# Kernel tuning notes

Measured on AMD Instinct MI355X. Metric: run time of the kernel, lower is better.

The kernel has to match this reference:

```python
import jax, jax.numpy as jnp
import numpy as np

NO_EDGE_OFFSET_T_NORM = 10.0
NO_EDGE_OFFSET_T_CONORM = -10.0

B, I, O = 64, 1024, 1024  # num_samples, in_features, out_features
N_EDGE_TYPES = 3          # 0=no_edge, 1=edge (identity), 2=negation (1-x)
N_OP_TYPES = 2            # 0=T_Norm.min, 1=T_Conorm.max


def setup_inputs() -> dict:
    key = jax.random.key(0)
    k1, k2, k3, k4 = jax.random.split(key, 4)
    # fuzzy inputs in [0, 1]
    x = jax.random.uniform(k1, (B, I), dtype=jnp.float32)
    # operator_type_counts is all-ones -> uniform multinomial over operator types (per node)
    op_idx = jax.random.randint(k2, (O,), 0, N_OP_TYPES, dtype=jnp.int32)
    # edge_type_count is all-ones -> uniform multinomial over edge types,
    # resampled per (sample, node, edge) exactly as the double python loop does
    et = jax.random.randint(k3, (B, O, I), 0, N_EDGE_TYPES, dtype=jnp.int32)
    # source fix-up: if every sampled index is 0 (all no_edge), force one random edge to type 1
    all_zero = jnp.all(et == 0, axis=-1)                      # [B, O]
    rand_pos = jax.random.randint(k4, (B, O), 0, I, dtype=jnp.int32)
    force = all_zero[:, :, None] & (jnp.arange(I)[None, None, :] == rand_pos[:, :, None])
    et = jnp.where(force, 1, et)
    return {"x": x, "edge_type_idx": et, "op_idx": op_idx}


def reference(x, edge_type_idx, op_idx):
    # x: [B, I] float; edge_type_idx: [B, O, I] int; op_idx: [O] int
    is_tnorm = (op_idx == 0)                                   # [O], op 0 = min (T_Norm)
    xb = x[:, None, :]                                         # [B, 1, I]
    # edge value: identity for edge/no_edge, 1-x for negation
    vals = jnp.where(edge_type_idx == 2, 1.0 - xb, xb)         # [B, O, I]
    # no_edge offset: +10 under t-norm (ignored by min), -10 under t-conorm (ignored by max)
    offset = jnp.where(is_tnorm[None, :, None], NO_EDGE_OFFSET_T_NORM, NO_EDGE_OFFSET_T_CONORM)
    vals = vals + jnp.where(edge_type_idx == 0, offset, 0.0)
    tn = jnp.min(vals, axis=-1)                                # [B, O] t-norm (min)
    tc = jnp.max(vals, axis=-1)                                # [B, O] t-conorm (max)
    return jnp.where(is_tnorm[None, :], tn, tc)
```

## Files before the change

### kernel.cpp

```cpp
#include <hip/hip_runtime.h>


constexpr int B = 64;
constexpr int I = 1024;
constexpr int O = 1024;
constexpr int ROWS_PER_WAVE = 8;
constexpr int BLOCKS = (B * O) / (ROWS_PER_WAVE * 4);

typedef int   iv4 __attribute__((ext_vector_type(4)));
typedef float fv4 __attribute__((ext_vector_type(4)));

__global__ __launch_bounds__(256) void ffcl_kernel(
    const float* __restrict__ x,
    const int*   __restrict__ et,
    const int*   __restrict__ op,
    float*       __restrict__ out)
{
    const int t    = threadIdx.x;
    const int wid  = t >> 6;
    const int lane = t & 63;
    const int wave = blockIdx.x * 4 + wid;
    const int r_base = wave * ROWS_PER_WAVE;
    const int b      = r_base >> 10;
    const int o_base = r_base & (O - 1);

    fv4 xv[4];
    #pragma unroll
    for (int j = 0; j < 4; ++j)
        xv[j] = *reinterpret_cast<const fv4*>(x + (size_t)b * I + j * 256 + lane * 4);

    float sgn[ROWS_PER_WAVE], off[ROWS_PER_WAVE];
    #pragma unroll
    for (int rr = 0; rr < ROWS_PER_WAVE; ++rr) {
        const bool is_t = (op[o_base + rr] == 0);
        sgn[rr] = is_t ? -1.0f : 1.0f;
        off[rr] = is_t ? 10.0f : -10.0f;
    }

    const iv4* pe = reinterpret_cast<const iv4*>(et + (size_t)r_base * I) + lane;

    float acc[ROWS_PER_WAVE];
    #pragma unroll
    for (int rr = 0; rr < ROWS_PER_WAVE; ++rr) acc[rr] = -3.0e38f;

    iv4 eA[4], eB[4];

#define PREFETCH(BUF, RR) { \
    _Pragma("unroll") \
    for (int j = 0; j < 4; ++j) BUF[j] = pe[(RR) * 256 + j * 64]; }

#define CONSUME(E, RR) { \
    _Pragma("unroll") \
    for (int j = 0; j < 4; ++j) { \
        float v; \
        v = (E[j].x == 2) ? 1.0f - xv[j].x : xv[j].x;  v += (E[j].x == 0) ? off[RR] : 0.0f;  acc[RR] = fmaxf(acc[RR], sgn[RR] * v); \
        v = (E[j].y == 2) ? 1.0f - xv[j].y : xv[j].y;  v += (E[j].y == 0) ? off[RR] : 0.0f;  acc[RR] = fmaxf(acc[RR], sgn[RR] * v); \
        v = (E[j].z == 2) ? 1.0f - xv[j].z : xv[j].z;  v += (E[j].z == 0) ? off[RR] : 0.0f;  acc[RR] = fmaxf(acc[RR], sgn[RR] * v); \
        v = (E[j].w == 2) ? 1.0f - xv[j].w : xv[j].w;  v += (E[j].w == 0) ? off[RR] : 0.0f;  acc[RR] = fmaxf(acc[RR], sgn[RR] * v); \
    } }

    PREFETCH(eA, 0)
    PREFETCH(eB, 1)  CONSUME(eA, 0)
    PREFETCH(eA, 2)  CONSUME(eB, 1)
    PREFETCH(eB, 3)  CONSUME(eA, 2)
    PREFETCH(eA, 4)  CONSUME(eB, 3)
    PREFETCH(eB, 5)  CONSUME(eA, 4)
    PREFETCH(eA, 6)  CONSUME(eB, 5)
    PREFETCH(eB, 7)  CONSUME(eA, 6)
                     CONSUME(eB, 7)

#undef PREFETCH
#undef CONSUME

    float keep = 0.0f;
    #pragma unroll
    for (int rr = 0; rr < ROWS_PER_WAVE; ++rr) {
        float a = acc[rr];
        #pragma unroll
        for (int s = 32; s > 0; s >>= 1)
            a = fmaxf(a, __shfl_xor(a, s, 64));
        if (lane == rr) keep = sgn[rr] * a;
    }
    if (lane < ROWS_PER_WAVE)
        out[r_base + lane] = keep;
}

extern "C" void kernel_launch(void* const* d_in, const int* in_sizes, int n_in,
                              void* d_out, int out_size, void* d_ws, size_t ws_size,
                              hipStream_t stream) {
    const float* x   = (const float*)d_in[0];
    const int*   et  = (const int*)d_in[1];
    const int*   op  = (const int*)d_in[2];
    float*       out = (float*)d_out;

    ffcl_kernel<<<BLOCKS, 256, 0, stream>>>(x, et, op, out);
}
```

Baseline: 357.2 us.

## Issue all edge-type loads upfront with nontemporal hints and halve rows per wave

Each wave now handles 4 rows instead of 8, which doubles the number of waves. Every wave issues all 16 of its vector loads of the edge-type tensor at the start, marked nontemporal, instead of running a two-buffer prefetch pipeline. The aim is more memory requests in flight on this streaming, bandwidth-bound read. The compute is also simplified: 1-x is precomputed once, and the per-op offset add is replaced by a sign multiply plus a -2 sentinel for no-edge entries. That sentinel only holds because every row is guaranteed at least one real edge, and holding 16 vectors in registers raises register pressure.

```diff
diff --git a/kernel.cpp b/kernel.cpp
--- a/kernel.cpp
+++ b/kernel.cpp
@@ -4,7 +4,7 @@
 constexpr int B = 64;
 constexpr int I = 1024;
 constexpr int O = 1024;
-constexpr int ROWS_PER_WAVE = 8;
+constexpr int ROWS_PER_WAVE = 4;
 constexpr int BLOCKS = (B * O) / (ROWS_PER_WAVE * 4);
 
 typedef int   iv4 __attribute__((ext_vector_type(4)));
@@ -16,65 +16,59 @@
     const int*   __restrict__ op,
     float*       __restrict__ out)
 {
-    const int t    = threadIdx.x;
-    const int wid  = t >> 6;
-    const int lane = t & 63;
-    const int wave = blockIdx.x * 4 + wid;
+    const int t      = threadIdx.x;
+    const int wid    = t >> 6;
+    const int lane   = t & 63;
+    const int wave   = blockIdx.x * 4 + wid;
     const int r_base = wave * ROWS_PER_WAVE;
     const int b      = r_base >> 10;
     const int o_base = r_base & (O - 1);
 
-    fv4 xv[4];
+    const iv4* pe = reinterpret_cast<const iv4*>(et + (size_t)r_base * I) + lane;
+
+    iv4 e[16];
     #pragma unroll
-    for (int j = 0; j < 4; ++j)
+    for (int rr = 0; rr < 4; ++rr)
+        #pragma unroll
+        for (int j = 0; j < 4; ++j)
+            e[rr * 4 + j] = __builtin_nontemporal_load(&pe[rr * 256 + j * 64]);
+
+    fv4 xv[4], qv[4];
+    #pragma unroll
+    for (int j = 0; j < 4; ++j) {
         xv[j] = *reinterpret_cast<const fv4*>(x + (size_t)b * I + j * 256 + lane * 4);
-
-    float sgn[ROWS_PER_WAVE], off[ROWS_PER_WAVE];
-    #pragma unroll
-    for (int rr = 0; rr < ROWS_PER_WAVE; ++rr) {
-        const bool is_t = (op[o_base + rr] == 0);
-        sgn[rr] = is_t ? -1.0f : 1.0f;
-        off[rr] = is_t ? 10.0f : -10.0f;
+        qv[j].x = 1.0f - xv[j].x;  qv[j].y = 1.0f - xv[j].y;
+        qv[j].z = 1.0f - xv[j].z;  qv[j].w = 1.0f - xv[j].w;
     }
 
-    const iv4* pe = reinterpret_cast<const iv4*>(et + (size_t)r_base * I) + lane;
+    float sgn[4];
+    #pragma unroll
+    for (int rr = 0; rr < 4; ++rr)
+        sgn[rr] = (op[o_base + rr] == 0) ? -1.0f : 1.0f;
 
-    float acc[ROWS_PER_WAVE];
+    float acc[4];
     #pragma unroll
-    for (int rr = 0; rr < ROWS_PER_WAVE; ++rr) acc[rr] = -3.0e38f;
+    for (int rr = 0; rr < 4; ++rr) acc[rr] = -3.0e38f;
 
-    iv4 eA[4], eB[4];
-
-#define PREFETCH(BUF, RR) { \
-    _Pragma("unroll") \
-    for (int j = 0; j < 4; ++j) BUF[j] = pe[(RR) * 256 + j * 64]; }
-
-#define CONSUME(E, RR) { \
-    _Pragma("unroll") \
-    for (int j = 0; j < 4; ++j) { \
-        float v; \
-        v = (E[j].x == 2) ? 1.0f - xv[j].x : xv[j].x;  v += (E[j].x == 0) ? off[RR] : 0.0f;  acc[RR] = fmaxf(acc[RR], sgn[RR] * v); \
-        v = (E[j].y == 2) ? 1.0f - xv[j].y : xv[j].y;  v += (E[j].y == 0) ? off[RR] : 0.0f;  acc[RR] = fmaxf(acc[RR], sgn[RR] * v); \
-        v = (E[j].z == 2) ? 1.0f - xv[j].z : xv[j].z;  v += (E[j].z == 0) ? off[RR] : 0.0f;  acc[RR] = fmaxf(acc[RR], sgn[RR] * v); \
-        v = (E[j].w == 2) ? 1.0f - xv[j].w : xv[j].w;  v += (E[j].w == 0) ? off[RR] : 0.0f;  acc[RR] = fmaxf(acc[RR], sgn[RR] * v); \
-    } }
-
-    PREFETCH(eA, 0)
-    PREFETCH(eB, 1)  CONSUME(eA, 0)
-    PREFETCH(eA, 2)  CONSUME(eB, 1)
-    PREFETCH(eB, 3)  CONSUME(eA, 2)
-    PREFETCH(eA, 4)  CONSUME(eB, 3)
-    PREFETCH(eB, 5)  CONSUME(eA, 4)
-    PREFETCH(eA, 6)  CONSUME(eB, 5)
-    PREFETCH(eB, 7)  CONSUME(eA, 6)
-                     CONSUME(eB, 7)
-
-#undef PREFETCH
-#undef CONSUME
+    #pragma unroll
+    for (int rr = 0; rr < 4; ++rr) {
+        const float s = sgn[rr];
+        #pragma unroll
+        for (int j = 0; j < 4; ++j) {
+            const iv4 ev = e[rr * 4 + j];
+            float c0, c1, c2, c3;
+            c0 = s * ((ev.x == 2) ? qv[j].x : xv[j].x);  c0 = (ev.x == 0) ? -2.0f : c0;
+            c1 = s * ((ev.y == 2) ? qv[j].y : xv[j].y);  c1 = (ev.y == 0) ? -2.0f : c1;
+            c2 = s * ((ev.z == 2) ? qv[j].z : xv[j].z);  c2 = (ev.z == 0) ? -2.0f : c2;
+            c3 = s * ((ev.w == 2) ? qv[j].w : xv[j].w);  c3 = (ev.w == 0) ? -2.0f : c3;
+            acc[rr] = fmaxf(fmaxf(acc[rr], c0), c1);
+            acc[rr] = fmaxf(fmaxf(acc[rr], c2), c3);
+        }
+    }
 
     float keep = 0.0f;
     #pragma unroll
-    for (int rr = 0; rr < ROWS_PER_WAVE; ++rr) {
+    for (int rr = 0; rr < 4; ++rr) {
         float a = acc[rr];
         #pragma unroll
         for (int s = 32; s > 0; s >>= 1)
```

Result: faster. 333.0 us (-6.8%).

## Deepen edge-type prefetch to five rows and simplify per-element min/max math

Applied to the files above, without the earlier changes.

Each wave now handles 16 rows instead of 8 and keeps five rows of edge-type loads in flight instead of two, to hide more memory latency on this bandwidth-bound read of 256MB of int32 edge types. The per-element math is rewritten: values are pre-multiplied by the sign, and no-edge entries become a -2 sentinel instead of an added offset. Each row is reduced and written right after it is consumed. The deeper buffering raises register pressure, and the grid now has half as many blocks.

```diff
diff --git a/kernel.cpp b/kernel.cpp
--- a/kernel.cpp
+++ b/kernel.cpp
@@ -4,13 +4,14 @@
 constexpr int B = 64;
 constexpr int I = 1024;
 constexpr int O = 1024;
-constexpr int ROWS_PER_WAVE = 8;
-constexpr int BLOCKS = (B * O) / (ROWS_PER_WAVE * 4);
+constexpr int ROWS_PER_WAVE  = 16;
+constexpr int WAVES_PER_BLOCK = 4;
+constexpr int BLOCKS = (B * O) / (ROWS_PER_WAVE * WAVES_PER_BLOCK);
 
 typedef int   iv4 __attribute__((ext_vector_type(4)));
 typedef float fv4 __attribute__((ext_vector_type(4)));
 
-__global__ __launch_bounds__(256) void ffcl_kernel(
+__global__ __launch_bounds__(256, 4) void ffcl_kernel(
     const float* __restrict__ x,
     const int*   __restrict__ et,
     const int*   __restrict__ op,
@@ -19,70 +20,65 @@
     const int t    = threadIdx.x;
     const int wid  = t >> 6;
     const int lane = t & 63;
-    const int wave = blockIdx.x * 4 + wid;
-    const int r_base = wave * ROWS_PER_WAVE;
-    const int b      = r_base >> 10;
-    const int o_base = r_base & (O - 1);
+    const int wave = blockIdx.x * WAVES_PER_BLOCK + wid;
+    const int r0   = wave * ROWS_PER_WAVE;
+    const int b    = r0 >> 10;
+    const int o0   = r0 & (O - 1);
 
     fv4 xv[4];
     #pragma unroll
     for (int j = 0; j < 4; ++j)
         xv[j] = *reinterpret_cast<const fv4*>(x + (size_t)b * I + j * 256 + lane * 4);
 
-    float sgn[ROWS_PER_WAVE], off[ROWS_PER_WAVE];
+    float sgn[ROWS_PER_WAVE];
     #pragma unroll
-    for (int rr = 0; rr < ROWS_PER_WAVE; ++rr) {
-        const bool is_t = (op[o_base + rr] == 0);
-        sgn[rr] = is_t ? -1.0f : 1.0f;
-        off[rr] = is_t ? 10.0f : -10.0f;
-    }
+    for (int rr = 0; rr < ROWS_PER_WAVE; ++rr)
+        sgn[rr] = (op[o0 + rr] == 0) ? -1.0f : 1.0f;
 
-    const iv4* pe = reinterpret_cast<const iv4*>(et + (size_t)r_base * I) + lane;
+    const iv4* pe = reinterpret_cast<const iv4*>(et + (size_t)r0 * I) + lane;
 
-    float acc[ROWS_PER_WAVE];
-    #pragma unroll
-    for (int rr = 0; rr < ROWS_PER_WAVE; ++rr) acc[rr] = -3.0e38f;
+    iv4 b0[4], b1[4], b2[4], b3[4], b4[4];
 
-    iv4 eA[4], eB[4];
-
-#define PREFETCH(BUF, RR) { \
-    _Pragma("unroll") \
+#define LOADROW(BUF, RR) { _Pragma("unroll") \
     for (int j = 0; j < 4; ++j) BUF[j] = pe[(RR) * 256 + j * 64]; }
 
-#define CONSUME(E, RR) { \
+#define CONSUME(BUF, RR) { \
+    const float s = sgn[RR]; \
+    float a = -2.0f; \
     _Pragma("unroll") \
     for (int j = 0; j < 4; ++j) { \
-        float v; \
-        v = (E[j].x == 2) ? 1.0f - xv[j].x : xv[j].x;  v += (E[j].x == 0) ? off[RR] : 0.0f;  acc[RR] = fmaxf(acc[RR], sgn[RR] * v); \
-        v = (E[j].y == 2) ? 1.0f - xv[j].y : xv[j].y;  v += (E[j].y == 0) ? off[RR] : 0.0f;  acc[RR] = fmaxf(acc[RR], sgn[RR] * v); \
-        v = (E[j].z == 2) ? 1.0f - xv[j].z : xv[j].z;  v += (E[j].z == 0) ? off[RR] : 0.0f;  acc[RR] = fmaxf(acc[RR], sgn[RR] * v); \
-        v = (E[j].w == 2) ? 1.0f - xv[j].w : xv[j].w;  v += (E[j].w == 0) ? off[RR] : 0.0f;  acc[RR] = fmaxf(acc[RR], sgn[RR] * v); \
-    } }
+        const iv4 ev = BUF[j]; \
+        const float t0 = s * xv[j].x, t1 = s * xv[j].y, t2 = s * xv[j].z, t3 = s * xv[j].w; \
+        float c0 = (ev.x == 2) ? s - t0 : t0;  c0 = (ev.x == 0) ? -2.0f : c0; \
+        float c1 = (ev.y == 2) ? s - t1 : t1;  c1 = (ev.y == 0) ? -2.0f : c1; \
+        float c2 = (ev.z == 2) ? s - t2 : t2;  c2 = (ev.z == 0) ? -2.0f : c2; \
+        float c3 = (ev.w == 2) ? s - t3 : t3;  c3 = (ev.w == 0) ? -2.0f : c3; \
+        a = fmaxf(fmaxf(a, c0), c1); \
+        a = fmaxf(fmaxf(a, c2), c3); \
+    } \
+    _Pragma("unroll") \
+    for (int sh = 32; sh > 0; sh >>= 1) a = fmaxf(a, __shfl_xor(a, sh, 64)); \
+    if (lane == 0) out[r0 + (RR)] = s * a; }
 
-    PREFETCH(eA, 0)
-    PREFETCH(eB, 1)  CONSUME(eA, 0)
-    PREFETCH(eA, 2)  CONSUME(eB, 1)
-    PREFETCH(eB, 3)  CONSUME(eA, 2)
-    PREFETCH(eA, 4)  CONSUME(eB, 3)
-    PREFETCH(eB, 5)  CONSUME(eA, 4)
-    PREFETCH(eA, 6)  CONSUME(eB, 5)
-    PREFETCH(eB, 7)  CONSUME(eA, 6)
-                     CONSUME(eB, 7)
-
-#undef PREFETCH
+    LOADROW(b0, 0) LOADROW(b1, 1) LOADROW(b2, 2) LOADROW(b3, 3) LOADROW(b4, 4)
+    CONSUME(b0, 0)   LOADROW(b0, 5)
+    CONSUME(b1, 1)   LOADROW(b1, 6)
+    CONSUME(b2, 2)   LOADROW(b2, 7)
+    CONSUME(b3, 3)   LOADROW(b3, 8)
+    CONSUME(b4, 4)   LOADROW(b4, 9)
+    CONSUME(b0, 5)   LOADROW(b0, 10)
+    CONSUME(b1, 6)   LOADROW(b1, 11)
+    CONSUME(b2, 7)   LOADROW(b2, 12)
+    CONSUME(b3, 8)   LOADROW(b3, 13)
+    CONSUME(b4, 9)   LOADROW(b4, 14)
+    CONSUME(b0, 10)  LOADROW(b0, 15)
+    CONSUME(b1, 11)
+    CONSUME(b2, 12)
+    CONSUME(b3, 13)
+    CONSUME(b4, 14)
+    CONSUME(b0, 15)
+#undef LOADROW
 #undef CONSUME
-
-    float keep = 0.0f;
-    #pragma unroll
-    for (int rr = 0; rr < ROWS_PER_WAVE; ++rr) {
-        float a = acc[rr];
-        #pragma unroll
-        for (int s = 32; s > 0; s >>= 1)
-            a = fmaxf(a, __shfl_xor(a, s, 64));
-        if (lane == rr) keep = sgn[rr] * a;
-    }
-    if (lane < ROWS_PER_WAVE)
-        out[r_base + lane] = keep;
 }
 
 extern "C" void kernel_launch(void* const* d_in, const int* in_sizes, int n_in,
```

Result: no change. 362.8 us (+1.6%).
